# Kernel optimization log

Measured on AMD Instinct MI355X. Metric: run time of the kernel, lower is better.

## Reference

```python
import jax, jax.numpy as jnp
import numpy as np

EPS = 1e-8
NCAND = 24  # 4 verts A + 4 verts B + 16 edge-pair intersections


def _cross(u, v):
    return u[..., 0] * v[..., 1] - u[..., 1] * v[..., 0]


def _get_corners(b):
    # b: [N,5] = (x, z, dx, dz, ry) -> BEV corners [N,4,2] (CCW for positive dims)
    x, z, dx, dz, ry = (b[:, i] for i in range(5))
    c, s = jnp.cos(ry), jnp.sin(ry)
    hx, hz = dx * 0.5, dz * 0.5
    lx = jnp.stack([hx, -hx, -hx, hx], axis=1)
    lz = jnp.stack([hz, hz, -hz, -hz], axis=1)
    cx = lx * c[:, None] - lz * s[:, None] + x[:, None]
    cz = lx * s[:, None] + lz * c[:, None] + z[:, None]
    return jnp.stack([cx, cz], axis=-1)


def _quad_area(C):
    # shoelace area of quad corners [N,4,2]
    nxt = jnp.roll(C, -1, axis=1)
    return 0.5 * jnp.abs(jnp.sum(_cross(C, nxt), axis=1))


def _points_in_quad(P, Q):
    # P: [N,4,2] query points, Q: [N,4,2] convex quad. True if inside (either orientation).
    q1 = Q[:, None, :, :]
    q2 = jnp.roll(Q, -1, axis=1)[:, None, :, :]
    s = _cross(q2 - q1, P[:, :, None, :] - q1)  # [N, 4 pts, 4 edges]
    return jnp.all(s >= -1e-6, axis=-1) | jnp.all(s <= 1e-6, axis=-1)


def _convex_intersect_area(A, B):
    # Area of intersection of two convex quads A,B: [N,4,2].
    N = A.shape[0]
    inA = _points_in_quad(A, B)  # A verts inside B
    inB = _points_in_quad(B, A)  # B verts inside A
    # all 4x4 edge-pair intersections
    a1, a2 = A[:, :, None, :], jnp.roll(A, -1, axis=1)[:, :, None, :]
    b1, b2 = B[:, None, :, :], jnp.roll(B, -1, axis=1)[:, None, :, :]
    da, db = a2 - a1, b2 - b1
    den = _cross(da, db)                       # [N,4,4]
    den_safe = jnp.where(jnp.abs(den) < EPS, 1.0, den)
    t = _cross(b1 - a1, db) / den_safe
    u = _cross(b1 - a1, da) / den_safe
    ok = (jnp.abs(den) >= EPS) & (t >= 0.0) & (t <= 1.0) & (u >= 0.0) & (u <= 1.0)
    ipts = a1 + t[..., None] * da              # [N,4,4,2]
    pts = jnp.concatenate([A, B, ipts.reshape(N, 16, 2)], axis=1)   # [N,24,2]
    mask = jnp.concatenate([inA, inB, ok.reshape(N, 16)], axis=1)   # [N,24]
    cnt = jnp.sum(mask, axis=1)
    ctr = jnp.sum(jnp.where(mask[..., None], pts, 0.0), axis=1) / jnp.maximum(cnt, 1).astype(pts.dtype)[:, None]
    rel = pts - ctr[:, None, :]
    relm = jnp.where(mask[..., None], rel, 1.0)  # avoid atan2(0,0)
    ang = jnp.where(mask, jnp.arctan2(relm[..., 1], relm[..., 0]), 1e9)
    order = jnp.argsort(ang, axis=1)
    rel_s = jnp.take_along_axis(rel, order[..., None], axis=1)       # valid pts first, CCW
    # shoelace over the first cnt points (cyclic)
    contrib = _cross(rel_s, jnp.roll(rel_s, -1, axis=1))             # [N,24]
    idx = jnp.arange(NCAND)[None, :]
    body = jnp.sum(jnp.where(idx < (cnt - 1)[:, None], contrib, 0.0), axis=1)
    li = jnp.broadcast_to(jnp.maximum(cnt - 1, 0)[:, None, None], (N, 1, 2))
    last = jnp.take_along_axis(rel_s, li, axis=1)[:, 0]
    closing = _cross(last, rel_s[:, 0])
    area = 0.5 * jnp.abs(body + closing)
    return jnp.where(cnt >= 3, area, 0.0)


def get_iou3d(pred_bboxes, target_bboxes):
    # Faithful vectorized port of the torch/shapely get_iou3d.
    min_h_a = -(pred_bboxes[:, 1] + pred_bboxes[:, 4] / 2)
    max_h_a = -(pred_bboxes[:, 1] - pred_bboxes[:, 4] / 2)
    min_h_b = -(target_bboxes[:, 1] + target_bboxes[:, 4] / 2)
    max_h_b = -(target_bboxes[:, 1] - target_bboxes[:, 4] / 2)
    h_overlap = jnp.clip(jnp.minimum(max_h_a, max_h_b) - jnp.maximum(min_h_a, min_h_b), 0.0)
    cols = jnp.array([0, 2, 3, 5, 6])
    pa = pred_bboxes[:, cols]
    pb = target_bboxes[:, cols]
    ca = _get_corners(pa)
    cb = _get_corners(pb)
    overlap = _convex_intersect_area(ca, cb)
    overlap3d = overlap * h_overlap
    area_a = _quad_area(ca)
    area_b = _quad_area(cb)
    # NOTE: original code indexes max_h_a[0]-min_h_a[0] (box 0's height) inside the loop;
    # replicated faithfully.
    h_a0 = max_h_a[0] - min_h_a[0]
    union3d = area_a * h_a0 + area_b * (max_h_b - min_h_b) - overlap3d
    return overlap3d / union3d


def setup_inputs() -> dict:
    N = 262144
    key = jax.random.key(0)
    ks = jax.random.split(key, 6)
    # target boxes: [x, y, z, d3, h, d5, ry]
    xz = jax.random.normal(ks[0], (N, 2), jnp.float32) * 20.0
    y = jax.random.normal(ks[1], (N, 1), jnp.float32) * 1.5
    dims = jax.random.uniform(ks[2], (N, 3), jnp.float32, 1.5, 4.5)
    ry = jax.random.uniform(ks[3], (N, 1), jnp.float32, -np.pi, np.pi)
    target = jnp.concatenate([xz[:, :1], y, xz[:, 1:], dims[:, :1], dims[:, 1:2], dims[:, 2:], ry], axis=1)
    noise = jax.random.normal(ks[4], (N, 7), jnp.float32) * jnp.array([0.5, 0.2, 0.5, 0.2, 0.2, 0.2, 0.1], jnp.float32)
    pred = target + noise
    return {"pred_bboxes": pred, "target_bboxes": target}


def reference(pred_bboxes, target_bboxes):
    return get_iou3d(pred_bboxes, target_bboxes)
```

## Files before the change

kernel.cpp:

```cpp
#include <hip/hip_runtime.h>
#include <math.h>

static __device__ __forceinline__ float xprod(float ux, float uz, float vx, float vz) {
    return ux * vz - uz * vx;
}

template<int NIN>
static __device__ __forceinline__ int clip_pass(
    const float (&inx)[8], const float (&inz)[8], int n,
    float ox, float oz, float ex, float ez,
    float (&outx)[8], float (&outz)[8])
{
    float d[NIN];
    #pragma unroll
    for (int i = 0; i < NIN; i++)
        d[i] = xprod(ex, ez, inx[i] - ox, inz[i] - oz);

    bool e0[NIN], e1[NIN];
    float qx[NIN], qz[NIN];
    int pos0[NIN], pos1[NIN];
    int c = 0;
    #pragma unroll
    for (int i = 0; i < NIN; i++) {
        bool active = (i < n);
        bool last = (i == n - 1);
        constexpr int NX = 0;
        (void)NX;
        float sx = last ? inx[0] : inx[(i + 1 < NIN) ? i + 1 : 0];
        float sz = last ? inz[0] : inz[(i + 1 < NIN) ? i + 1 : 0];
        float ds = last ? d[0]   : d[(i + 1 < NIN) ? i + 1 : 0];
        bool ins  = d[i] >= 0.0f;
        bool inss = ds   >= 0.0f;
        bool crossing = active && (ins != inss);
        float denom = d[i] - ds;
        float t = __fdividef(d[i], (denom == 0.0f) ? 1.0f : denom);
        qx[i] = inx[i] + t * (sx - inx[i]);
        qz[i] = inz[i] + t * (sz - inz[i]);
        e0[i] = active && ins;
        e1[i] = crossing;
        pos0[i] = c; c += e0[i] ? 1 : 0;
        pos1[i] = c; c += e1[i] ? 1 : 0;
    }

    #pragma unroll
    for (int j = 0; j <= NIN && j < 8; j++) {
        float vx = 0.0f, vz = 0.0f;
        #pragma unroll
        for (int i = 0; i < NIN; i++) {
            bool s0 = e0[i] && (pos0[i] == j);
            vx = s0 ? inx[i] : vx;
            vz = s0 ? inz[i] : vz;
            bool s1 = e1[i] && (pos1[i] == j);
            vx = s1 ? qx[i] : vx;
            vz = s1 ? qz[i] : vz;
        }
        outx[j] = vx; outz[j] = vz;
    }
    return c;
}

__global__ __launch_bounds__(256) void iou3d_kernel(
    const float* __restrict__ pred,
    const float* __restrict__ tgt,
    float* __restrict__ out,
    int N)
{
    int i = blockIdx.x * blockDim.x + threadIdx.x;
    if (i >= N) return;

    const float* pa = pred + (long)i * 7;
    const float* pb = tgt  + (long)i * 7;

    float a_x  = pa[0], a_y = pa[1], a_z = pa[2];
    float a_dx = pa[3], a_dy = pa[4], a_dz = pa[5], a_ry = pa[6];
    float b_x  = pb[0], b_y = pb[1], b_z = pb[2];
    float b_dx = pb[3], b_dy = pb[4], b_dz = pb[5], b_ry = pb[6];

    float min_h_a = -(a_y + a_dy * 0.5f);
    float max_h_a = -(a_y - a_dy * 0.5f);
    float min_h_b = -(b_y + b_dy * 0.5f);
    float max_h_b = -(b_y - b_dy * 0.5f);
    float h_ov = fmaxf(fminf(max_h_a, max_h_b) - fmaxf(min_h_a, min_h_b), 0.0f);

    float y0 = pred[1], dy0 = pred[4];
    float h_a0 = (-(y0 - dy0 * 0.5f)) - (-(y0 + dy0 * 0.5f));

    float Axc[4], Azc[4], Bxc[4], Bzc[4];
    {
        float c = __cosf(a_ry), s = __sinf(a_ry);
        float hx = a_dx * 0.5f, hz = a_dz * 0.5f;
        const float lx[4] = { hx, -hx, -hx, hx };
        const float lz[4] = { hz, hz, -hz, -hz };
        #pragma unroll
        for (int k = 0; k < 4; k++) {
            Axc[k] = lx[k] * c - lz[k] * s + a_x;
            Azc[k] = lx[k] * s + lz[k] * c + a_z;
        }
    }
    {
        float c = __cosf(b_ry), s = __sinf(b_ry);
        float hx = b_dx * 0.5f, hz = b_dz * 0.5f;
        const float lx[4] = { hx, -hx, -hx, hx };
        const float lz[4] = { hz, hz, -hz, -hz };
        #pragma unroll
        for (int k = 0; k < 4; k++) {
            Bxc[k] = lx[k] * c - lz[k] * s + b_x;
            Bzc[k] = lx[k] * s + lz[k] * c + b_z;
        }
    }

    float area_a = 0.0f, area_b = 0.0f;
    #pragma unroll
    for (int k = 0; k < 4; k++) {
        int kn = (k + 1) & 3;
        area_a += xprod(Axc[k], Azc[k], Axc[kn], Azc[kn]);
        area_b += xprod(Bxc[k], Bzc[k], Bxc[kn], Bzc[kn]);
    }
    area_a = 0.5f * fabsf(area_a);
    area_b = 0.5f * fabsf(area_b);

    float Px[8], Pz[8], Qx[8], Qz[8];
    #pragma unroll
    for (int k = 0; k < 8; k++) { Px[k] = 0.f; Pz[k] = 0.f; Qx[k] = 0.f; Qz[k] = 0.f; }
    #pragma unroll
    for (int k = 0; k < 4; k++) { Px[k] = Axc[k]; Pz[k] = Azc[k]; }
    int n = 4;

    n = clip_pass<4>(Px, Pz, n, Bxc[0], Bzc[0], Bxc[1] - Bxc[0], Bzc[1] - Bzc[0], Qx, Qz);
    n = clip_pass<5>(Qx, Qz, n, Bxc[1], Bzc[1], Bxc[2] - Bxc[1], Bzc[2] - Bzc[1], Px, Pz);
    n = clip_pass<6>(Px, Pz, n, Bxc[2], Bzc[2], Bxc[3] - Bxc[2], Bzc[3] - Bzc[2], Qx, Qz);
    n = clip_pass<7>(Qx, Qz, n, Bxc[3], Bzc[3], Bxc[0] - Bxc[3], Bzc[0] - Bzc[3], Px, Pz);

    float area2 = 0.0f;
    #pragma unroll
    for (int j = 0; j < 8; j++) {
        bool act = (j < n);
        bool last = (j == n - 1);
        float sx = last ? Px[0] : Px[(j + 1 < 8) ? j + 1 : 0];
        float sz = last ? Pz[0] : Pz[(j + 1 < 8) ? j + 1 : 0];
        float c = xprod(Px[j], Pz[j], sx, sz);
        area2 += act ? c : 0.0f;
    }
    float area = 0.5f * fabsf(area2);
    area = (n >= 3) ? area : 0.0f;

    float overlap3d = area * h_ov;
    float union3d = area_a * h_a0 + area_b * (max_h_b - min_h_b) - overlap3d;
    out[i] = overlap3d / union3d;
}

extern "C" void kernel_launch(void* const* d_in, const int* in_sizes, int n_in,
                              void* d_out, int out_size, void* d_ws, size_t ws_size,
                              hipStream_t stream) {
    const float* pred = (const float*)d_in[0];
    const float* tgt  = (const float*)d_in[1];
    float* out = (float*)d_out;
    int N = in_sizes[0] / 7;
    int block = 256;
    int grid = (N + block - 1) / block;
    hipLaunchKernelGGL(iou3d_kernel, dim3(grid), dim3(block), 0, stream,
                       pred, tgt, out, N);
}
```

Baseline: 74.64 us.

## Replace Sutherland-Hodgman clipping with per-edge boundary contribution area formula

```diff
diff --git a/kernel.cpp b/kernel.cpp
--- a/kernel.cpp
+++ b/kernel.cpp
@@ -5,58 +5,51 @@
     return ux * vz - uz * vx;
 }
 
-template<int NIN>
-static __device__ __forceinline__ int clip_pass(
-    const float (&inx)[8], const float (&inz)[8], int n,
-    float ox, float oz, float ex, float ez,
-    float (&outx)[8], float (&outz)[8])
+static __device__ __forceinline__ float edge_contrib(
+    const float (&Pxc)[4], const float (&Pzc)[4],
+    const float (&Qxc)[4], const float (&Qzc)[4])
 {
-    float d[NIN];
+    float ex[4], ez[4], ec[4];
     #pragma unroll
-    for (int i = 0; i < NIN; i++)
-        d[i] = xprod(ex, ez, inx[i] - ox, inz[i] - oz);
-
-    bool e0[NIN], e1[NIN];
-    float qx[NIN], qz[NIN];
-    int pos0[NIN], pos1[NIN];
-    int c = 0;
-    #pragma unroll
-    for (int i = 0; i < NIN; i++) {
-        bool active = (i < n);
-        bool last = (i == n - 1);
-        constexpr int NX = 0;
-        (void)NX;
-        float sx = last ? inx[0] : inx[(i + 1 < NIN) ? i + 1 : 0];
-        float sz = last ? inz[0] : inz[(i + 1 < NIN) ? i + 1 : 0];
-        float ds = last ? d[0]   : d[(i + 1 < NIN) ? i + 1 : 0];
-        bool ins  = d[i] >= 0.0f;
-        bool inss = ds   >= 0.0f;
-        bool crossing = active && (ins != inss);
-        float denom = d[i] - ds;
-        float t = __fdividef(d[i], (denom == 0.0f) ? 1.0f : denom);
-        qx[i] = inx[i] + t * (sx - inx[i]);
-        qz[i] = inz[i] + t * (sz - inz[i]);
-        e0[i] = active && ins;
-        e1[i] = crossing;
-        pos0[i] = c; c += e0[i] ? 1 : 0;
-        pos1[i] = c; c += e1[i] ? 1 : 0;
+    for (int j = 0; j < 4; j++) {
+        int jn = (j + 1) & 3;
+        ex[j] = Qxc[jn] - Qxc[j];
+        ez[j] = Qzc[jn] - Qzc[j];
+        ec[j] = ex[j] * Qzc[j] - ez[j] * Qxc[j];
     }
 
+    float d[4][4];
     #pragma unroll
-    for (int j = 0; j <= NIN && j < 8; j++) {
-        float vx = 0.0f, vz = 0.0f;
+    for (int i = 0; i < 4; i++) {
         #pragma unroll
-        for (int i = 0; i < NIN; i++) {
-            bool s0 = e0[i] && (pos0[i] == j);
-            vx = s0 ? inx[i] : vx;
-            vz = s0 ? inz[i] : vz;
-            bool s1 = e1[i] && (pos1[i] == j);
-            vx = s1 ? qx[i] : vx;
-            vz = s1 ? qz[i] : vz;
+        for (int j = 0; j < 4; j++) {
+            d[i][j] = ex[j] * Pzc[i] - ez[j] * Pxc[i] - ec[j];
         }
-        outx[j] = vx; outz[j] = vz;
     }
-    return c;
+
+    float acc = 0.0f;
+    #pragma unroll
+    for (int i = 0; i < 4; i++) {
+        int in_ = (i + 1) & 3;
+        float t_lo = 0.0f, t_hi = 1.0f;
+        #pragma unroll
+        for (int j = 0; j < 4; j++) {
+            float d0 = d[i][j], d1 = d[in_][j];
+            float den = d0 - d1;
+            float t = __fdividef(d0, (den == 0.0f) ? 1.0f : den);
+            t_lo = (den < 0.0f) ? fmaxf(t_lo, t) : t_lo;
+            t_hi = (den > 0.0f) ? fminf(t_hi, t) : t_hi;
+            t_lo = (den == 0.0f && d0 < 0.0f) ? 1e9f : t_lo;
+        }
+        bool valid = t_lo < t_hi;
+        float ax = Pxc[i], az = Pzc[i];
+        float dx = Pxc[in_] - ax, dz = Pzc[in_] - az;
+        float p0x = ax + t_lo * dx, p0z = az + t_lo * dz;
+        float p1x = ax + t_hi * dx, p1z = az + t_hi * dz;
+        float c = xprod(p0x, p0z, p1x, p1z);
+        acc += valid ? c : 0.0f;
+    }
+    return acc;
 }
 
 __global__ __launch_bounds__(256) void iou3d_kernel(
@@ -85,6 +78,11 @@
     float y0 = pred[1], dy0 = pred[4];
     float h_a0 = (-(y0 - dy0 * 0.5f)) - (-(y0 + dy0 * 0.5f));
 
+    float mx = 0.5f * (a_x + b_x);
+    float mz = 0.5f * (a_z + b_z);
+    float ax0 = a_x - mx, az0 = a_z - mz;
+    float bx0 = b_x - mx, bz0 = b_z - mz;
+
     float Axc[4], Azc[4], Bxc[4], Bzc[4];
     {
         float c = __cosf(a_ry), s = __sinf(a_ry);
@@ -93,8 +91,8 @@
         const float lz[4] = { hz, hz, -hz, -hz };
         #pragma unroll
         for (int k = 0; k < 4; k++) {
-            Axc[k] = lx[k] * c - lz[k] * s + a_x;
-            Azc[k] = lx[k] * s + lz[k] * c + a_z;
+            Axc[k] = lx[k] * c - lz[k] * s + ax0;
+            Azc[k] = lx[k] * s + lz[k] * c + az0;
         }
     }
     {
@@ -104,45 +102,17 @@
         const float lz[4] = { hz, hz, -hz, -hz };
         #pragma unroll
         for (int k = 0; k < 4; k++) {
-            Bxc[k] = lx[k] * c - lz[k] * s + b_x;
-            Bzc[k] = lx[k] * s + lz[k] * c + b_z;
+            Bxc[k] = lx[k] * c - lz[k] * s + bx0;
+            Bzc[k] = lx[k] * s + lz[k] * c + bz0;
         }
     }
 
-    float area_a = 0.0f, area_b = 0.0f;
-    #pragma unroll
-    for (int k = 0; k < 4; k++) {
-        int kn = (k + 1) & 3;
-        area_a += xprod(Axc[k], Azc[k], Axc[kn], Azc[kn]);
-        area_b += xprod(Bxc[k], Bzc[k], Bxc[kn], Bzc[kn]);
-    }
-    area_a = 0.5f * fabsf(area_a);
-    area_b = 0.5f * fabsf(area_b);
+    float area_a = a_dx * a_dz;
+    float area_b = b_dx * b_dz;
 
-    float Px[8], Pz[8], Qx[8], Qz[8];
-    #pragma unroll
-    for (int k = 0; k < 8; k++) { Px[k] = 0.f; Pz[k] = 0.f; Qx[k] = 0.f; Qz[k] = 0.f; }
-    #pragma unroll
-    for (int k = 0; k < 4; k++) { Px[k] = Axc[k]; Pz[k] = Azc[k]; }
-    int n = 4;
-
-    n = clip_pass<4>(Px, Pz, n, Bxc[0], Bzc[0], Bxc[1] - Bxc[0], Bzc[1] - Bzc[0], Qx, Qz);
-    n = clip_pass<5>(Qx, Qz, n, Bxc[1], Bzc[1], Bxc[2] - Bxc[1], Bzc[2] - Bzc[1], Px, Pz);
-    n = clip_pass<6>(Px, Pz, n, Bxc[2], Bzc[2], Bxc[3] - Bxc[2], Bzc[3] - Bzc[2], Qx, Qz);
-    n = clip_pass<7>(Qx, Qz, n, Bxc[3], Bzc[3], Bxc[0] - Bxc[3], Bzc[0] - Bzc[3], Px, Pz);
-
-    float area2 = 0.0f;
-    #pragma unroll
-    for (int j = 0; j < 8; j++) {
-        bool act = (j < n);
-        bool last = (j == n - 1);
-        float sx = last ? Px[0] : Px[(j + 1 < 8) ? j + 1 : 0];
-        float sz = last ? Pz[0] : Pz[(j + 1 < 8) ? j + 1 : 0];
-        float c = xprod(Px[j], Pz[j], sx, sz);
-        area2 += act ? c : 0.0f;
-    }
-    float area = 0.5f * fabsf(area2);
-    area = (n >= 3) ? area : 0.0f;
+    float acc = edge_contrib(Axc, Azc, Bxc, Bzc)
+              + edge_contrib(Bxc, Bzc, Axc, Azc);
+    float area = 0.5f * fabsf(acc);
 
     float overlap3d = area * h_ov;
     float union3d = area_a * h_a0 + area_b * (max_h_b - min_h_b) - overlap3d;
```

Result: faster. 69.27 us (-7.2%).
